# Kernel tuning notes

Measured on AMD Instinct MI355X. Metric: run time of the kernel, lower is better.

The kernel has to match this reference:

```python
import jax, jax.numpy as jnp
import numpy as np


def setup_inputs() -> dict:
    key = jax.random.key(0)
    ks = jax.random.split(key, 16)
    B, S, H = 512, 128, 256
    f32 = jnp.float32
    inputs = jax.random.normal(ks[0], (B, S, 2), f32)
    # xavier-normal-ish init (gain/sqrt(fan_in+fan_out) approximated by small scale)
    def xn(k, shape):
        fan = shape[0] + shape[1]
        return jax.random.normal(k, shape, f32) * np.sqrt(2.0 / fan)
    return {
        "inputs": inputs,
        "W0": xn(ks[1], (H, 2)),   "b0": jnp.zeros((H,), f32),
        "W1": xn(ks[2], (H, H)),   "b1": jnp.zeros((H,), f32),
        "W2": xn(ks[3], (H, H)),   "b2": jnp.zeros((H,), f32),
        "W3": xn(ks[4], (H, H)),   "b3": jnp.zeros((H,), f32),
        "W4": xn(ks[5], (1, H)),   "b4": jnp.zeros((1,), f32),
        "log_growth_rate": jax.random.normal(ks[6], (), f32),
        "log_carrying_capacity": jax.random.normal(ks[7], (), f32),
        "log_initial_loss": jax.random.normal(ks[8], (), f32),
        "in_mean": jnp.array([0.5, 50.0], f32),
        "in_std": jnp.array([0.2, 30.0], f32),
        "tgt_mean": jnp.array([0.8], f32),
        "tgt_std": jnp.array([0.1], f32),
    }


def reference(inputs, W0, b0, W1, b1, W2, b2, W3, b3, W4, b4,
              log_growth_rate, log_carrying_capacity, log_initial_loss,
              in_mean, in_std, tgt_mean, tgt_std):
    B, S = inputs.shape[0], inputs.shape[1]
    # PDE parameters (Verhulst logistic growth)
    r = jnp.exp(-log_growth_rate)
    K = 0.2 + (1.0 - 0.2) * jax.nn.sigmoid(log_carrying_capacity)  # carrying capacity in [0.2, 1]
    C = 0.0 + (0.1 - 0.0) * jax.nn.sigmoid(log_initial_loss)       # initial loss in [0, 0.1]

    # split state feature s and time t, standardize per-column
    s = inputs[..., 0:1].reshape(-1, 1)  # [N,1]
    t = inputs[..., 1:2].reshape(-1, 1)  # [N,1]
    s_norm = (s - in_mean[0:1]) / (in_std[0:1] + 1e-8)
    t_norm = (t - in_mean[1:2]) / (in_std[1:2] + 1e-8)

    Ws = (W0, W1, W2, W3, W4)
    bs = (b0, b1, b2, b3, b4)

    def mlp(x):  # [N,2] -> [N,1], tanh MLP
        h = x
        for W, b in zip(Ws[:-1], bs[:-1]):
            h = jnp.tanh(h @ W.T + b)
        return h @ Ws[-1].T + bs[-1]

    def u_of(tn):  # U(s_norm, tn), inverse-standardized targets
        return mlp(jnp.concatenate([s_norm, tn], axis=-1)) * tgt_std + tgt_mean

    ones = jnp.ones_like(t_norm)

    def uf_of(tn):
        # U and U_t = dU/dt_norm (forward-mode; each point depends on its own scalar t)
        U, U_dot = jax.jvp(u_of, (tn,), (ones,))
        U_t = U_dot.sum(-1, keepdims=True)
        G = r * (U - C) * (1.0 - (U - C) / (K - C))  # Verhulst
        return U, U_t - G  # (U, F)

    # second derivative w.r.t. t_norm: F_t = U_tt - G_t
    (U, F), (_, F_t) = jax.jvp(uf_of, (t_norm,), (ones,))

    shp = (B, S, 1)
    return U.reshape(shp), F.reshape(shp), F_t.reshape(shp)
```

## Files before the change

### kernel.cpp

```cpp
#include <hip/hip_runtime.h>
#include <hip/hip_bf16.h>
#include <math.h>

typedef short s8v __attribute__((ext_vector_type(8)));
typedef float f4v __attribute__((ext_vector_type(4)));

#define HH 256
#define TP 16
#define NTHREADS 256
#define KSTR 520
#define TSTR 4160
#define NTILES 3
#define PLANE (NTILES * TSTR)

__device__ __forceinline__ unsigned short bf_rne(float x){
    union{float f;unsigned u;}v; v.f=x;
    unsigned r = v.u + 0x7FFFu + ((v.u >> 16) & 1u);
    return (unsigned short)(r >> 16);
}
__device__ __forceinline__ unsigned pack_rne2(float a, float b){
    union { __hip_bfloat162 h; unsigned u; } v;
    v.h = __float22bfloat162_rn(float2{a, b});
    return v.u;
}

__global__ __launch_bounds__(256)
void prep_weights(const float* __restrict__ W1, const float* __restrict__ W2,
                  const float* __restrict__ W3, const float* __restrict__ W0,
                  const float* __restrict__ b0, const float* __restrict__ W4,
                  unsigned short* __restrict__ wsB, float* __restrict__ wsF)
{
    int t = blockIdx.x * 256 + threadIdx.x;
    if (t < 24576) {
        int layer = t >> 13;
        int rem = t & 8191;
        int l  = rem & 63;
        int ks = (rem >> 6) & 7;
        int nt = rem >> 9;
        const float* W = (layer == 0) ? W1 : (layer == 1) ? W2 : W3;
        int n_out = nt * 16 + (l & 15);
        int quad  = l >> 4;
        const float* row = W + n_out * HH;
        s8v hi;
        #pragma unroll
        for (int j = 0; j < 8; ++j) {
            int n_in = quad * 64 + (j & 3) * 16 + ((j >> 2) << 3) + ks;
            hi[j] = (short)bf_rne(row[n_in]);
        }
        int dst = ((nt * 8 + ks) * 64 + l) * 8;
        *(s8v*)(wsB + layer * 65536 + dst) = hi;
    } else if (t < 24832) {
        int n = t - 24576;
        int pos = ((n & 7) * 4 + (n >> 6)) * 8 + ((n >> 4) & 3) + 4 * ((n >> 3) & 1);
        wsF[pos]       = W0[2 * n];
        wsF[256 + pos] = W0[2 * n + 1];
        wsF[512 + pos] = b0[n];
        wsF[768 + pos] = W4[n];
    }
}

__global__ __launch_bounds__(NTHREADS, 4)
void capnn_mfma(const float* __restrict__ inp,
                const float* __restrict__ b1, const float* __restrict__ b2,
                const float* __restrict__ b3, const float* __restrict__ b4,
                const float* __restrict__ W4raw,
                const float* __restrict__ lgr, const float* __restrict__ lcc,
                const float* __restrict__ lil,
                const float* __restrict__ imean, const float* __restrict__ istd,
                const float* __restrict__ tmean, const float* __restrict__ tstd,
                const unsigned short* __restrict__ wsW,
                const float* __restrict__ wsF,
                float* __restrict__ out, int N)
{
    __shared__ __align__(16) unsigned short Ahi[PLANE];
    __shared__ float sn_sh[TP], tn_sh[TP];
    __shared__ float head_part[TP * 3 * 4];

    const int tid  = threadIdx.x;
    const int lane = tid & 63;
    const int w    = tid >> 6;
    const int m16  = lane & 15;
    const int q    = lane >> 4;
    const int pbase = blockIdx.x * TP;

    const float* __restrict__ w00p = wsF;
    const float* __restrict__ w01p = wsF + 256;
    const float* __restrict__ b0p  = wsF + 512;

    if (tid < TP) {
        int pg = pbase + tid;
        float s = 0.f, t = 0.f;
        if (pg < N) { s = inp[2 * pg]; t = inp[2 * pg + 1]; }
        sn_sh[tid] = (s - imean[0]) / (istd[0] + 1e-8f);
        tn_sh[tid] = (t - imean[1]) / (istd[1] + 1e-8f);
    }
    __syncthreads();

    {
        const int l  = lane;
        const int p16 = l & 15, quad = l >> 4;
        const float sn = sn_sh[p16], tn = tn_sh[p16];
        #pragma unroll
        for (int g2 = 0; g2 < 2; ++g2) {
            const int ks = w + 4 * g2;
            const int pos = (ks * 4 + quad) * 8;
            float4 wA0 = *(const float4*)(w00p + pos);
            float4 wA1 = *(const float4*)(w00p + pos + 4);
            float4 wB0 = *(const float4*)(w01p + pos);
            float4 wB1 = *(const float4*)(w01p + pos + 4);
            float4 bb0 = *(const float4*)(b0p + pos);
            float4 bb1 = *(const float4*)(b0p + pos + 4);
            float w00v[8] = {wA0.x,wA0.y,wA0.z,wA0.w,wA1.x,wA1.y,wA1.z,wA1.w};
            float w01v[8] = {wB0.x,wB0.y,wB0.z,wB0.w,wB1.x,wB1.y,wB1.z,wB1.w};
            float b0v[8]  = {bb0.x,bb0.y,bb0.z,bb0.w,bb1.x,bb1.y,bb1.z,bb1.w};
            const int base = ks * KSTR + l * 8;
            float av[8], d1v[8], d2v[8];
            #pragma unroll
            for (int j = 0; j < 8; ++j) {
                float z = fmaf(w00v[j], sn, fmaf(w01v[j], tn, b0v[j]));
                float e = __expf(2.f * z);
                float a = 1.f - 2.f * __builtin_amdgcn_rcpf(e + 1.f);
                float g = 1.f - a * a;
                float d1 = g * w01v[j];
                float d2 = -2.f * a * d1 * w01v[j];
                av[j] = a; d1v[j] = d1; d2v[j] = d2;
            }
            #pragma unroll
            for (int s = 0; s < 3; ++s) {
                const float* V = (s == 0) ? av : (s == 1) ? d1v : d2v;
                int4 hi4;
                hi4.x = (int)pack_rne2(V[0], V[1]);
                hi4.y = (int)pack_rne2(V[2], V[3]);
                hi4.z = (int)pack_rne2(V[4], V[5]);
                hi4.w = (int)pack_rne2(V[6], V[7]);
                *(int4*)&Ahi[s * TSTR + base] = hi4;
            }
        }
    }
    __syncthreads();

    for (int L = 0; L < 3; ++L) {
        const unsigned short* __restrict__ Wlh = wsW + L * 65536;
        const float* __restrict__ bL = (L == 0) ? b1 : (L == 1) ? b2 : b3;

        f4v acc[NTILES][4];
        #pragma unroll
        for (int i = 0; i < 4; ++i) {
            float bias = bL[w * 64 + i * 16 + m16];
            acc[0][i] = (f4v){bias, bias, bias, bias};
            acc[1][i] = (f4v){0.f, 0.f, 0.f, 0.f};
            acc[2][i] = (f4v){0.f, 0.f, 0.f, 0.f};
        }

        __builtin_amdgcn_s_setprio(1);
        #pragma unroll
        for (int ks = 0; ks < 8; ++ks) {
            s8v ah[NTILES];
            const int aoff = ks * KSTR + lane * 8;
            #pragma unroll
            for (int t = 0; t < NTILES; ++t)
                ah[t] = *(const s8v*)&Ahi[t * TSTR + aoff];
            #pragma unroll
            for (int i = 0; i < 4; ++i) {
                const int off = (((w * 4 + i) * 8 + ks) * 64 + lane) * 8;
                s8v bh = *(const s8v*)(Wlh + off);
                #pragma unroll
                for (int t = 0; t < NTILES; ++t)
                    acc[t][i] = __builtin_amdgcn_mfma_f32_16x16x32_bf16(ah[t], bh, acc[t][i], 0, 0, 0);
            }
        }
        __builtin_amdgcn_s_setprio(0);

        if (L < 2) {
            __syncthreads();
            const int ksw  = m16 & 7;
            const int hsel = m16 >> 3;
            const int wbase = ksw * KSTR + (16 * w + q * 4) * 8 + 4 * hsel;
            #pragma unroll
            for (int r = 0; r < 4; ++r) {
                float Av[3][4];
                #pragma unroll
                for (int i = 0; i < 4; ++i) {
                    float z  = acc[0][i][r];
                    float z1 = acc[1][i][r];
                    float z2 = acc[2][i][r];
                    float e = __expf(2.f * z);
                    float a = 1.f - 2.f * __builtin_amdgcn_rcpf(e + 1.f);
                    float g = 1.f - a * a;
                    float d1 = g * z1;
                    float d2 = fmaf(g, z2, -2.f * a * d1 * z1);
                    Av[0][i] = a; Av[1][i] = d1; Av[2][i] = d2;
                }
                #pragma unroll
                for (int s = 0; s < 3; ++s) {
                    int2 hi2;
                    hi2.x = (int)pack_rne2(Av[s][0], Av[s][1]);
                    hi2.y = (int)pack_rne2(Av[s][2], Av[s][3]);
                    *(int2*)&Ahi[s * TSTR + wbase + r * 8] = hi2;
                }
            }
            __syncthreads();
        } else {
            float w4v[4];
            #pragma unroll
            for (int i = 0; i < 4; ++i) w4v[i] = W4raw[w * 64 + i * 16 + m16];

            float hp[3][4];
            #pragma unroll
            for (int s = 0; s < 3; ++s)
                #pragma unroll
                for (int r = 0; r < 4; ++r) hp[s][r] = 0.f;
            #pragma unroll
            for (int r = 0; r < 4; ++r) {
                #pragma unroll
                for (int i = 0; i < 4; ++i) {
                    float z  = acc[0][i][r];
                    float z1 = acc[1][i][r];
                    float z2 = acc[2][i][r];
                    float e = __expf(2.f * z);
                    float a = 1.f - 2.f * __builtin_amdgcn_rcpf(e + 1.f);
                    float g = 1.f - a * a;
                    float d1 = g * z1;
                    float d2 = fmaf(g, z2, -2.f * a * d1 * z1);
                    hp[0][r] = fmaf(w4v[i], a,  hp[0][r]);
                    hp[1][r] = fmaf(w4v[i], d1, hp[1][r]);
                    hp[2][r] = fmaf(w4v[i], d2, hp[2][r]);
                }
            }
            #pragma unroll
            for (int m = 1; m < 16; m <<= 1) {
                #pragma unroll
                for (int s = 0; s < 3; ++s)
                    #pragma unroll
                    for (int r = 0; r < 4; ++r)
                        hp[s][r] += __shfl_xor(hp[s][r], m);
            }
            if (m16 == 0) {
                #pragma unroll
                for (int s = 0; s < 3; ++s)
                    #pragma unroll
                    for (int r = 0; r < 4; ++r)
                        head_part[(s * TP + q * 4 + r) * 4 + w] = hp[s][r];
            }
            __syncthreads();
        }
    }

    if (tid < TP) {
        float sv = 0.f, s1v = 0.f, s2v = 0.f;
        #pragma unroll
        for (int ww = 0; ww < 4; ++ww) {
            sv  += head_part[(0 * TP + tid) * 4 + ww];
            s1v += head_part[(1 * TP + tid) * 4 + ww];
            s2v += head_part[(2 * TP + tid) * 4 + ww];
        }
        int pg = pbase + tid;
        if (pg < N) {
            float r_  = expf(-lgr[0]);
            float Kc  = 0.2f + 0.8f / (1.f + expf(-lcc[0]));
            float Cc  = 0.1f / (1.f + expf(-lil[0]));
            float kci = 1.f / (Kc - Cc);
            float ts = tstd[0], tm = tmean[0];
            float U   = (sv + b4[0]) * ts + tm;
            float Ut  = s1v * ts;
            float Utt = s2v * ts;
            float Um  = U - Cc;
            float G   = r_ * Um * (1.f - Um * kci);
            float Gt  = r_ * Ut * (1.f - 2.f * Um * kci);
            out[pg]         = U;
            out[N + pg]     = Ut - G;
            out[2 * N + pg] = Utt - Gt;
        }
    }
}

extern "C" void kernel_launch(void* const* d_in, const int* in_sizes, int n_in,
                              void* d_out, int out_size, void* d_ws, size_t ws_size,
                              hipStream_t stream) {
    const float* inp   = (const float*)d_in[0];
    const float* W0    = (const float*)d_in[1];
    const float* b0    = (const float*)d_in[2];
    const float* W1    = (const float*)d_in[3];
    const float* b1    = (const float*)d_in[4];
    const float* W2    = (const float*)d_in[5];
    const float* b2    = (const float*)d_in[6];
    const float* W3    = (const float*)d_in[7];
    const float* b3    = (const float*)d_in[8];
    const float* W4    = (const float*)d_in[9];
    const float* b4    = (const float*)d_in[10];
    const float* lgr   = (const float*)d_in[11];
    const float* lcc   = (const float*)d_in[12];
    const float* lil   = (const float*)d_in[13];
    const float* imean = (const float*)d_in[14];
    const float* istd  = (const float*)d_in[15];
    const float* tmean = (const float*)d_in[16];
    const float* tstd  = (const float*)d_in[17];

    unsigned short* wsB = (unsigned short*)d_ws;
    float* wsF = (float*)((char*)d_ws + 393216);

    const int N = in_sizes[0] / 2;
    const int gridMain = (N + TP - 1) / TP;

    hipLaunchKernelGGL(prep_weights, dim3(97), dim3(256), 0, stream,
                       W1, W2, W3, W0, b0, W4, wsB, wsF);
    hipLaunchKernelGGL(capnn_mfma, dim3(gridMain), dim3(NTHREADS), 0, stream,
                       inp, b1, b2, b3, b4, W4,
                       lgr, lcc, lil, imean, istd, tmean, tstd,
                       wsB, wsF, (float*)d_out, N);
}
```

Before: 180.4 us.

## Process two point groups per block and interleave MFMA with tanh transforms

Each block now handles 32 points as two 16-point groups with separate LDS planes and accumulators. The layers are software-pipelined so the MFMA work of one group overlaps the tanh/derivative transform of the other. Each layer's weights are also reused across both groups, so B-operand loads per point are halved. In exchange the block uses twice the LDS and more registers, and the occupancy hint drops from 4 to 3 blocks per CU.

```diff
diff --git a/kernel.cpp b/kernel.cpp
--- a/kernel.cpp
+++ b/kernel.cpp
@@ -6,7 +6,7 @@
 typedef float f4v __attribute__((ext_vector_type(4)));
 
 #define HH 256
-#define TP 16
+#define TP 32
 #define NTHREADS 256
 #define KSTR 520
 #define TSTR 4160
@@ -59,7 +59,108 @@
     }
 }
 
-__global__ __launch_bounds__(NTHREADS, 4)
+#define MFMA_LAYER(ACC, PB, WLH, BL) do {                                   \
+    _Pragma("unroll")                                                       \
+    for (int i_ = 0; i_ < 4; ++i_) {                                        \
+        float bias_ = (BL)[w * 64 + i_ * 16 + m16];                         \
+        (ACC)[0][i_] = (f4v){bias_, bias_, bias_, bias_};                   \
+        (ACC)[1][i_] = (f4v){0.f, 0.f, 0.f, 0.f};                           \
+        (ACC)[2][i_] = (f4v){0.f, 0.f, 0.f, 0.f};                           \
+    }                                                                       \
+    __builtin_amdgcn_s_setprio(1);                                          \
+    _Pragma("unroll")                                                       \
+    for (int ks_ = 0; ks_ < 8; ++ks_) {                                     \
+        s8v ah_[NTILES];                                                    \
+        const int aoff_ = (PB) + ks_ * KSTR + lane * 8;                     \
+        _Pragma("unroll")                                                   \
+        for (int t_ = 0; t_ < NTILES; ++t_)                                 \
+            ah_[t_] = *(const s8v*)&Ahi[t_ * TSTR + aoff_];                 \
+        _Pragma("unroll")                                                   \
+        for (int i_ = 0; i_ < 4; ++i_) {                                    \
+            const int off_ = (((w * 4 + i_) * 8 + ks_) * 64 + lane) * 8;    \
+            s8v bh_ = *(const s8v*)((WLH) + off_);                          \
+            _Pragma("unroll")                                               \
+            for (int t_ = 0; t_ < NTILES; ++t_)                             \
+                (ACC)[t_][i_] = __builtin_amdgcn_mfma_f32_16x16x32_bf16(    \
+                    ah_[t_], bh_, (ACC)[t_][i_], 0, 0, 0);                  \
+        }                                                                   \
+    }                                                                       \
+    __builtin_amdgcn_s_setprio(0);                                          \
+} while (0)
+
+#define TRANSFORM(ACC, PB) do {                                             \
+    const int ksw_  = m16 & 7;                                              \
+    const int hsel_ = m16 >> 3;                                             \
+    const int wbase_ = (PB) + ksw_ * KSTR + (16 * w + q * 4) * 8 + 4 * hsel_; \
+    _Pragma("unroll")                                                       \
+    for (int r_ = 0; r_ < 4; ++r_) {                                        \
+        float Av_[3][4];                                                    \
+        _Pragma("unroll")                                                   \
+        for (int i_ = 0; i_ < 4; ++i_) {                                    \
+            float z_  = (ACC)[0][i_][r_];                                   \
+            float z1_ = (ACC)[1][i_][r_];                                   \
+            float z2_ = (ACC)[2][i_][r_];                                   \
+            float e_ = __expf(2.f * z_);                                    \
+            float a_ = 1.f - 2.f * __builtin_amdgcn_rcpf(e_ + 1.f);         \
+            float g_ = 1.f - a_ * a_;                                       \
+            float d1_ = g_ * z1_;                                           \
+            float d2_ = fmaf(g_, z2_, -2.f * a_ * d1_ * z1_);               \
+            Av_[0][i_] = a_; Av_[1][i_] = d1_; Av_[2][i_] = d2_;            \
+        }                                                                   \
+        _Pragma("unroll")                                                   \
+        for (int s_ = 0; s_ < 3; ++s_) {                                    \
+            int2 hi2_;                                                      \
+            hi2_.x = (int)pack_rne2(Av_[s_][0], Av_[s_][1]);                \
+            hi2_.y = (int)pack_rne2(Av_[s_][2], Av_[s_][3]);                \
+            *(int2*)&Ahi[s_ * TSTR + wbase_ + r_ * 8] = hi2_;               \
+        }                                                                   \
+    }                                                                       \
+} while (0)
+
+#define HEAD(ACC, G) do {                                                   \
+    float w4v_[4];                                                          \
+    _Pragma("unroll")                                                       \
+    for (int i_ = 0; i_ < 4; ++i_) w4v_[i_] = W4raw[w * 64 + i_ * 16 + m16];\
+    float hp_[3][4];                                                        \
+    _Pragma("unroll")                                                       \
+    for (int s_ = 0; s_ < 3; ++s_)                                          \
+        _Pragma("unroll")                                                   \
+        for (int r_ = 0; r_ < 4; ++r_) hp_[s_][r_] = 0.f;                   \
+    _Pragma("unroll")                                                       \
+    for (int r_ = 0; r_ < 4; ++r_) {                                        \
+        _Pragma("unroll")                                                   \
+        for (int i_ = 0; i_ < 4; ++i_) {                                    \
+            float z_  = (ACC)[0][i_][r_];                                   \
+            float z1_ = (ACC)[1][i_][r_];                                   \
+            float z2_ = (ACC)[2][i_][r_];                                   \
+            float e_ = __expf(2.f * z_);                                    \
+            float a_ = 1.f - 2.f * __builtin_amdgcn_rcpf(e_ + 1.f);         \
+            float g_ = 1.f - a_ * a_;                                       \
+            float d1_ = g_ * z1_;                                           \
+            float d2_ = fmaf(g_, z2_, -2.f * a_ * d1_ * z1_);               \
+            hp_[0][r_] = fmaf(w4v_[i_], a_,  hp_[0][r_]);                   \
+            hp_[1][r_] = fmaf(w4v_[i_], d1_, hp_[1][r_]);                   \
+            hp_[2][r_] = fmaf(w4v_[i_], d2_, hp_[2][r_]);                   \
+        }                                                                   \
+    }                                                                       \
+    _Pragma("unroll")                                                       \
+    for (int m_ = 1; m_ < 16; m_ <<= 1) {                                   \
+        _Pragma("unroll")                                                   \
+        for (int s_ = 0; s_ < 3; ++s_)                                      \
+            _Pragma("unroll")                                               \
+            for (int r_ = 0; r_ < 4; ++r_)                                  \
+                hp_[s_][r_] += __shfl_xor(hp_[s_][r_], m_);                 \
+    }                                                                       \
+    if (m16 == 0) {                                                         \
+        _Pragma("unroll")                                                   \
+        for (int s_ = 0; s_ < 3; ++s_)                                      \
+            _Pragma("unroll")                                               \
+            for (int r_ = 0; r_ < 4; ++r_)                                  \
+                head_part[G][(s_ * 16 + q * 4 + r_) * 4 + w] = hp_[s_][r_]; \
+    }                                                                       \
+} while (0)
+
+__global__ __launch_bounds__(NTHREADS, 3)
 void capnn_mfma(const float* __restrict__ inp,
                 const float* __restrict__ b1, const float* __restrict__ b2,
                 const float* __restrict__ b3, const float* __restrict__ b4,
@@ -72,9 +173,9 @@
                 const float* __restrict__ wsF,
                 float* __restrict__ out, int N)
 {
-    __shared__ __align__(16) unsigned short Ahi[PLANE];
+    __shared__ __align__(16) unsigned short Ahi[2 * PLANE];
     __shared__ float sn_sh[TP], tn_sh[TP];
-    __shared__ float head_part[TP * 3 * 4];
+    __shared__ float head_part[2][16 * 3 * 4];
 
     const int tid  = threadIdx.x;
     const int lane = tid & 63;
@@ -99,7 +200,6 @@
     {
         const int l  = lane;
         const int p16 = l & 15, quad = l >> 4;
-        const float sn = sn_sh[p16], tn = tn_sh[p16];
         #pragma unroll
         for (int g2 = 0; g2 < 2; ++g2) {
             const int ks = w + 4 * g2;
@@ -114,145 +214,70 @@
             float w01v[8] = {wB0.x,wB0.y,wB0.z,wB0.w,wB1.x,wB1.y,wB1.z,wB1.w};
             float b0v[8]  = {bb0.x,bb0.y,bb0.z,bb0.w,bb1.x,bb1.y,bb1.z,bb1.w};
             const int base = ks * KSTR + l * 8;
-            float av[8], d1v[8], d2v[8];
             #pragma unroll
-            for (int j = 0; j < 8; ++j) {
-                float z = fmaf(w00v[j], sn, fmaf(w01v[j], tn, b0v[j]));
-                float e = __expf(2.f * z);
-                float a = 1.f - 2.f * __builtin_amdgcn_rcpf(e + 1.f);
-                float g = 1.f - a * a;
-                float d1 = g * w01v[j];
-                float d2 = -2.f * a * d1 * w01v[j];
-                av[j] = a; d1v[j] = d1; d2v[j] = d2;
-            }
-            #pragma unroll
-            for (int s = 0; s < 3; ++s) {
-                const float* V = (s == 0) ? av : (s == 1) ? d1v : d2v;
-                int4 hi4;
-                hi4.x = (int)pack_rne2(V[0], V[1]);
-                hi4.y = (int)pack_rne2(V[2], V[3]);
-                hi4.z = (int)pack_rne2(V[4], V[5]);
-                hi4.w = (int)pack_rne2(V[6], V[7]);
-                *(int4*)&Ahi[s * TSTR + base] = hi4;
+            for (int h = 0; h < 2; ++h) {
+                const float sn = sn_sh[h * 16 + p16];
+                const float tn = tn_sh[h * 16 + p16];
+                float av[8], d1v[8], d2v[8];
+                #pragma unroll
+                for (int j = 0; j < 8; ++j) {
+                    float z = fmaf(w00v[j], sn, fmaf(w01v[j], tn, b0v[j]));
+                    float e = __expf(2.f * z);
+                    float a = 1.f - 2.f * __builtin_amdgcn_rcpf(e + 1.f);
+                    float g = 1.f - a * a;
+                    float d1 = g * w01v[j];
+                    float d2 = -2.f * a * d1 * w01v[j];
+                    av[j] = a; d1v[j] = d1; d2v[j] = d2;
+                }
+                #pragma unroll
+                for (int s = 0; s < 3; ++s) {
+                    const float* V = (s == 0) ? av : (s == 1) ? d1v : d2v;
+                    int4 hi4;
+                    hi4.x = (int)pack_rne2(V[0], V[1]);
+                    hi4.y = (int)pack_rne2(V[2], V[3]);
+                    hi4.z = (int)pack_rne2(V[4], V[5]);
+                    hi4.w = (int)pack_rne2(V[6], V[7]);
+                    *(int4*)&Ahi[h * PLANE + s * TSTR + base] = hi4;
+                }
             }
         }
     }
     __syncthreads();
 
-    for (int L = 0; L < 3; ++L) {
-        const unsigned short* __restrict__ Wlh = wsW + L * 65536;
-        const float* __restrict__ bL = (L == 0) ? b1 : (L == 1) ? b2 : b3;
-
-        f4v acc[NTILES][4];
-        #pragma unroll
-        for (int i = 0; i < 4; ++i) {
-            float bias = bL[w * 64 + i * 16 + m16];
-            acc[0][i] = (f4v){bias, bias, bias, bias};
-            acc[1][i] = (f4v){0.f, 0.f, 0.f, 0.f};
-            acc[2][i] = (f4v){0.f, 0.f, 0.f, 0.f};
-        }
-
-        __builtin_amdgcn_s_setprio(1);
-        #pragma unroll
-        for (int ks = 0; ks < 8; ++ks) {
-            s8v ah[NTILES];
-            const int aoff = ks * KSTR + lane * 8;
-            #pragma unroll
-            for (int t = 0; t < NTILES; ++t)
-                ah[t] = *(const s8v*)&Ahi[t * TSTR + aoff];
-            #pragma unroll
-            for (int i = 0; i < 4; ++i) {
-                const int off = (((w * 4 + i) * 8 + ks) * 64 + lane) * 8;
-                s8v bh = *(const s8v*)(Wlh + off);
-                #pragma unroll
-                for (int t = 0; t < NTILES; ++t)
-                    acc[t][i] = __builtin_amdgcn_mfma_f32_16x16x32_bf16(ah[t], bh, acc[t][i], 0, 0, 0);
-            }
-        }
-        __builtin_amdgcn_s_setprio(0);
-
-        if (L < 2) {
-            __syncthreads();
-            const int ksw  = m16 & 7;
-            const int hsel = m16 >> 3;
-            const int wbase = ksw * KSTR + (16 * w + q * 4) * 8 + 4 * hsel;
-            #pragma unroll
-            for (int r = 0; r < 4; ++r) {
-                float Av[3][4];
-                #pragma unroll
-                for (int i = 0; i < 4; ++i) {
-                    float z  = acc[0][i][r];
-                    float z1 = acc[1][i][r];
-                    float z2 = acc[2][i][r];
-                    float e = __expf(2.f * z);
-                    float a = 1.f - 2.f * __builtin_amdgcn_rcpf(e + 1.f);
-                    float g = 1.f - a * a;
-                    float d1 = g * z1;
-                    float d2 = fmaf(g, z2, -2.f * a * d1 * z1);
-                    Av[0][i] = a; Av[1][i] = d1; Av[2][i] = d2;
-                }
-                #pragma unroll
-                for (int s = 0; s < 3; ++s) {
-                    int2 hi2;
-                    hi2.x = (int)pack_rne2(Av[s][0], Av[s][1]);
-                    hi2.y = (int)pack_rne2(Av[s][2], Av[s][3]);
-                    *(int2*)&Ahi[s * TSTR + wbase + r * 8] = hi2;
-                }
-            }
-            __syncthreads();
-        } else {
-            float w4v[4];
-            #pragma unroll
-            for (int i = 0; i < 4; ++i) w4v[i] = W4raw[w * 64 + i * 16 + m16];
-
-            float hp[3][4];
-            #pragma unroll
-            for (int s = 0; s < 3; ++s)
-                #pragma unroll
-                for (int r = 0; r < 4; ++r) hp[s][r] = 0.f;
-            #pragma unroll
-            for (int r = 0; r < 4; ++r) {
-                #pragma unroll
-                for (int i = 0; i < 4; ++i) {
-                    float z  = acc[0][i][r];
-                    float z1 = acc[1][i][r];
-                    float z2 = acc[2][i][r];
-                    float e = __expf(2.f * z);
-                    float a = 1.f - 2.f * __builtin_amdgcn_rcpf(e + 1.f);
-                    float g = 1.f - a * a;
-                    float d1 = g * z1;
-                    float d2 = fmaf(g, z2, -2.f * a * d1 * z1);
-                    hp[0][r] = fmaf(w4v[i], a,  hp[0][r]);
-                    hp[1][r] = fmaf(w4v[i], d1, hp[1][r]);
-                    hp[2][r] = fmaf(w4v[i], d2, hp[2][r]);
-                }
-            }
-            #pragma unroll
-            for (int m = 1; m < 16; m <<= 1) {
-                #pragma unroll
-                for (int s = 0; s < 3; ++s)
-                    #pragma unroll
-                    for (int r = 0; r < 4; ++r)
-                        hp[s][r] += __shfl_xor(hp[s][r], m);
-            }
-            if (m16 == 0) {
-                #pragma unroll
-                for (int s = 0; s < 3; ++s)
-                    #pragma unroll
-                    for (int r = 0; r < 4; ++r)
-                        head_part[(s * TP + q * 4 + r) * 4 + w] = hp[s][r];
-            }
-            __syncthreads();
-        }
-    }
+    f4v accA[NTILES][4], accB[NTILES][4];
+    const unsigned short* __restrict__ W1h = wsW;
+    const unsigned short* __restrict__ W2h = wsW + 65536;
+    const unsigned short* __restrict__ W3h = wsW + 131072;
+
+    MFMA_LAYER(accA, 0, W1h, b1);
+    __syncthreads();
+    MFMA_LAYER(accB, PLANE, W1h, b1);
+    TRANSFORM(accA, 0);
+    __syncthreads();
+    MFMA_LAYER(accA, 0, W2h, b2);
+    TRANSFORM(accB, PLANE);
+    __syncthreads();
+    MFMA_LAYER(accB, PLANE, W2h, b2);
+    TRANSFORM(accA, 0);
+    __syncthreads();
+    MFMA_LAYER(accA, 0, W3h, b3);
+    TRANSFORM(accB, PLANE);
+    __syncthreads();
+    MFMA_LAYER(accB, PLANE, W3h, b3);
+    HEAD(accA, 0);
+    __syncthreads();
+    HEAD(accB, 1);
+    __syncthreads();
 
     if (tid < TP) {
+        const int g = tid >> 4;
+        const int p = tid & 15;
         float sv = 0.f, s1v = 0.f, s2v = 0.f;
         #pragma unroll
         for (int ww = 0; ww < 4; ++ww) {
-            sv  += head_part[(0 * TP + tid) * 4 + ww];
-            s1v += head_part[(1 * TP + tid) * 4 + ww];
-            s2v += head_part[(2 * TP + tid) * 4 + ww];
+            sv  += head_part[g][(0 * 16 + p) * 4 + ww];
+            s1v += head_part[g][(1 * 16 + p) * 4 + ww];
+            s2v += head_part[g][(2 * 16 + p) * 4 + ww];
         }
         int pg = pbase + tid;
         if (pg < N) {
```

New measurement: 195.5 us. +8.4%, slower.

## Double-buffer activation LDS planes and prefetch weight fragments across k-steps

Applied to the files above, without the earlier changes.

Splits the activation tile in shared memory into two ping-pong planes so each layer reads from one plane and writes the next layer's activations to the other. This removes the barrier that used to sit between the MFMA loop and the tanh transform. The MFMA loop now loads the next k-step's weight fragments from global memory before issuing the current step's MFMAs, to hide load latency. Launch bounds drop from 4 to 3 blocks per CU and shared memory per block doubles, which trades occupancy for more registers and fewer syncs.

```diff
diff --git a/kernel.cpp b/kernel.cpp
--- a/kernel.cpp
+++ b/kernel.cpp
@@ -59,7 +59,77 @@
     }
 }
 
-__global__ __launch_bounds__(NTHREADS, 4)
+#define MFMA_LAYER(ACC, RB, WLH, BL) do {                                   \
+    _Pragma("unroll")                                                       \
+    for (int i_ = 0; i_ < 4; ++i_) {                                        \
+        float bias_ = (BL)[w * 64 + i_ * 16 + m16];                         \
+        (ACC)[0][i_] = (f4v){bias_, bias_, bias_, bias_};                   \
+        (ACC)[1][i_] = (f4v){0.f, 0.f, 0.f, 0.f};                          \
+        (ACC)[2][i_] = (f4v){0.f, 0.f, 0.f, 0.f};                          \
+    }                                                                       \
+    s8v bc0_ = *(const s8v*)((WLH) + (((w * 4 + 0) * 8 + 0) * 64 + lane) * 8); \
+    s8v bc1_ = *(const s8v*)((WLH) + (((w * 4 + 1) * 8 + 0) * 64 + lane) * 8); \
+    s8v bc2_ = *(const s8v*)((WLH) + (((w * 4 + 2) * 8 + 0) * 64 + lane) * 8); \
+    s8v bc3_ = *(const s8v*)((WLH) + (((w * 4 + 3) * 8 + 0) * 64 + lane) * 8); \
+    __builtin_amdgcn_s_setprio(1);                                          \
+    _Pragma("unroll")                                                       \
+    for (int ks_ = 0; ks_ < 8; ++ks_) {                                     \
+        const int kn_ = (ks_ < 7) ? ks_ + 1 : ks_;                          \
+        s8v bn0_ = *(const s8v*)((WLH) + (((w * 4 + 0) * 8 + kn_) * 64 + lane) * 8); \
+        s8v bn1_ = *(const s8v*)((WLH) + (((w * 4 + 1) * 8 + kn_) * 64 + lane) * 8); \
+        s8v bn2_ = *(const s8v*)((WLH) + (((w * 4 + 2) * 8 + kn_) * 64 + lane) * 8); \
+        s8v bn3_ = *(const s8v*)((WLH) + (((w * 4 + 3) * 8 + kn_) * 64 + lane) * 8); \
+        const int aoff_ = (RB) + ks_ * KSTR + lane * 8;                     \
+        s8v ah0_ = *(const s8v*)&Ahi[0 * TSTR + aoff_];                     \
+        s8v ah1_ = *(const s8v*)&Ahi[1 * TSTR + aoff_];                     \
+        s8v ah2_ = *(const s8v*)&Ahi[2 * TSTR + aoff_];                     \
+        (ACC)[0][0] = __builtin_amdgcn_mfma_f32_16x16x32_bf16(ah0_, bc0_, (ACC)[0][0], 0, 0, 0); \
+        (ACC)[1][0] = __builtin_amdgcn_mfma_f32_16x16x32_bf16(ah1_, bc0_, (ACC)[1][0], 0, 0, 0); \
+        (ACC)[2][0] = __builtin_amdgcn_mfma_f32_16x16x32_bf16(ah2_, bc0_, (ACC)[2][0], 0, 0, 0); \
+        (ACC)[0][1] = __builtin_amdgcn_mfma_f32_16x16x32_bf16(ah0_, bc1_, (ACC)[0][1], 0, 0, 0); \
+        (ACC)[1][1] = __builtin_amdgcn_mfma_f32_16x16x32_bf16(ah1_, bc1_, (ACC)[1][1], 0, 0, 0); \
+        (ACC)[2][1] = __builtin_amdgcn_mfma_f32_16x16x32_bf16(ah2_, bc1_, (ACC)[2][1], 0, 0, 0); \
+        (ACC)[0][2] = __builtin_amdgcn_mfma_f32_16x16x32_bf16(ah0_, bc2_, (ACC)[0][2], 0, 0, 0); \
+        (ACC)[1][2] = __builtin_amdgcn_mfma_f32_16x16x32_bf16(ah1_, bc2_, (ACC)[1][2], 0, 0, 0); \
+        (ACC)[2][2] = __builtin_amdgcn_mfma_f32_16x16x32_bf16(ah2_, bc2_, (ACC)[2][2], 0, 0, 0); \
+        (ACC)[0][3] = __builtin_amdgcn_mfma_f32_16x16x32_bf16(ah0_, bc3_, (ACC)[0][3], 0, 0, 0); \
+        (ACC)[1][3] = __builtin_amdgcn_mfma_f32_16x16x32_bf16(ah1_, bc3_, (ACC)[1][3], 0, 0, 0); \
+        (ACC)[2][3] = __builtin_amdgcn_mfma_f32_16x16x32_bf16(ah2_, bc3_, (ACC)[2][3], 0, 0, 0); \
+        bc0_ = bn0_; bc1_ = bn1_; bc2_ = bn2_; bc3_ = bn3_;                 \
+    }                                                                       \
+    __builtin_amdgcn_s_setprio(0);                                          \
+} while (0)
+
+#define TRANSFORM(ACC, WB) do {                                             \
+    const int ksw_  = m16 & 7;                                              \
+    const int hsel_ = m16 >> 3;                                             \
+    const int wbase_ = (WB) + ksw_ * KSTR + (16 * w + q * 4) * 8 + 4 * hsel_; \
+    _Pragma("unroll")                                                       \
+    for (int r_ = 0; r_ < 4; ++r_) {                                        \
+        float Av_[3][4];                                                    \
+        _Pragma("unroll")                                                   \
+        for (int i_ = 0; i_ < 4; ++i_) {                                    \
+            float z_  = (ACC)[0][i_][r_];                                   \
+            float z1_ = (ACC)[1][i_][r_];                                   \
+            float z2_ = (ACC)[2][i_][r_];                                   \
+            float e_ = __expf(2.f * z_);                                    \
+            float a_ = 1.f - 2.f * __builtin_amdgcn_rcpf(e_ + 1.f);         \
+            float g_ = 1.f - a_ * a_;                                       \
+            float d1_ = g_ * z1_;                                           \
+            float d2_ = fmaf(g_, z2_, -2.f * a_ * d1_ * z1_);               \
+            Av_[0][i_] = a_; Av_[1][i_] = d1_; Av_[2][i_] = d2_;            \
+        }                                                                   \
+        _Pragma("unroll")                                                   \
+        for (int s_ = 0; s_ < 3; ++s_) {                                    \
+            int2 hi2_;                                                      \
+            hi2_.x = (int)pack_rne2(Av_[s_][0], Av_[s_][1]);                \
+            hi2_.y = (int)pack_rne2(Av_[s_][2], Av_[s_][3]);                \
+            *(int2*)&Ahi[s_ * TSTR + wbase_ + r_ * 8] = hi2_;               \
+        }                                                                   \
+    }                                                                       \
+} while (0)
+
+__global__ __launch_bounds__(NTHREADS, 3)
 void capnn_mfma(const float* __restrict__ inp,
                 const float* __restrict__ b1, const float* __restrict__ b2,
                 const float* __restrict__ b3, const float* __restrict__ b4,
@@ -72,7 +142,7 @@
                 const float* __restrict__ wsF,
                 float* __restrict__ out, int N)
 {
-    __shared__ __align__(16) unsigned short Ahi[PLANE];
+    __shared__ __align__(16) unsigned short Ahi[2 * PLANE];
     __shared__ float sn_sh[TP], tn_sh[TP];
     __shared__ float head_part[TP * 3 * 4];
 
@@ -139,112 +209,64 @@
     }
     __syncthreads();
 
-    for (int L = 0; L < 3; ++L) {
-        const unsigned short* __restrict__ Wlh = wsW + L * 65536;
-        const float* __restrict__ bL = (L == 0) ? b1 : (L == 1) ? b2 : b3;
-
-        f4v acc[NTILES][4];
-        #pragma unroll
-        for (int i = 0; i < 4; ++i) {
-            float bias = bL[w * 64 + i * 16 + m16];
-            acc[0][i] = (f4v){bias, bias, bias, bias};
-            acc[1][i] = (f4v){0.f, 0.f, 0.f, 0.f};
-            acc[2][i] = (f4v){0.f, 0.f, 0.f, 0.f};
-        }
-
-        __builtin_amdgcn_s_setprio(1);
-        #pragma unroll
-        for (int ks = 0; ks < 8; ++ks) {
-            s8v ah[NTILES];
-            const int aoff = ks * KSTR + lane * 8;
-            #pragma unroll
-            for (int t = 0; t < NTILES; ++t)
-                ah[t] = *(const s8v*)&Ahi[t * TSTR + aoff];
+    f4v acc[NTILES][4];
+    const unsigned short* __restrict__ W1h = wsW;
+    const unsigned short* __restrict__ W2h = wsW + 65536;
+    const unsigned short* __restrict__ W3h = wsW + 131072;
+
+    MFMA_LAYER(acc, 0, W1h, b1);
+    TRANSFORM(acc, PLANE);
+    __syncthreads();
+
+    MFMA_LAYER(acc, PLANE, W2h, b2);
+    TRANSFORM(acc, 0);
+    __syncthreads();
+
+    MFMA_LAYER(acc, 0, W3h, b3);
+    {
+        float w4v[4];
+        #pragma unroll
+        for (int i = 0; i < 4; ++i) w4v[i] = W4raw[w * 64 + i * 16 + m16];
+
+        float hp[3][4];
+        #pragma unroll
+        for (int s = 0; s < 3; ++s)
+            #pragma unroll
+            for (int r = 0; r < 4; ++r) hp[s][r] = 0.f;
+        #pragma unroll
+        for (int r = 0; r < 4; ++r) {
             #pragma unroll
             for (int i = 0; i < 4; ++i) {
-                const int off = (((w * 4 + i) * 8 + ks) * 64 + lane) * 8;
-                s8v bh = *(const s8v*)(Wlh + off);
-                #pragma unroll
-                for (int t = 0; t < NTILES; ++t)
-                    acc[t][i] = __builtin_amdgcn_mfma_f32_16x16x32_bf16(ah[t], bh, acc[t][i], 0, 0, 0);
+                float z  = acc[0][i][r];
+                float z1 = acc[1][i][r];
+                float z2 = acc[2][i][r];
+                float e = __expf(2.f * z);
+                float a = 1.f - 2.f * __builtin_amdgcn_rcpf(e + 1.f);
+                float g = 1.f - a * a;
+                float d1 = g * z1;
+                float d2 = fmaf(g, z2, -2.f * a * d1 * z1);
+                hp[0][r] = fmaf(w4v[i], a,  hp[0][r]);
+                hp[1][r] = fmaf(w4v[i], d1, hp[1][r]);
+                hp[2][r] = fmaf(w4v[i], d2, hp[2][r]);
             }
         }
-        __builtin_amdgcn_s_setprio(0);
-
-        if (L < 2) {
-            __syncthreads();
-            const int ksw  = m16 & 7;
-            const int hsel = m16 >> 3;
-            const int wbase = ksw * KSTR + (16 * w + q * 4) * 8 + 4 * hsel;
-            #pragma unroll
-            for (int r = 0; r < 4; ++r) {
-                float Av[3][4];
-                #pragma unroll
-                for (int i = 0; i < 4; ++i) {
-                    float z  = acc[0][i][r];
-                    float z1 = acc[1][i][r];
-                    float z2 = acc[2][i][r];
-                    float e = __expf(2.f * z);
-                    float a = 1.f - 2.f * __builtin_amdgcn_rcpf(e + 1.f);
-                    float g = 1.f - a * a;
-                    float d1 = g * z1;
-                    float d2 = fmaf(g, z2, -2.f * a * d1 * z1);
-                    Av[0][i] = a; Av[1][i] = d1; Av[2][i] = d2;
-                }
-                #pragma unroll
-                for (int s = 0; s < 3; ++s) {
-                    int2 hi2;
-                    hi2.x = (int)pack_rne2(Av[s][0], Av[s][1]);
-                    hi2.y = (int)pack_rne2(Av[s][2], Av[s][3]);
-                    *(int2*)&Ahi[s * TSTR + wbase + r * 8] = hi2;
-                }
-            }
-            __syncthreads();
-        } else {
-            float w4v[4];
-            #pragma unroll
-            for (int i = 0; i < 4; ++i) w4v[i] = W4raw[w * 64 + i * 16 + m16];
-
-            float hp[3][4];
+        #pragma unroll
+        for (int m = 1; m < 16; m <<= 1) {
             #pragma unroll
             for (int s = 0; s < 3; ++s)
                 #pragma unroll
-                for (int r = 0; r < 4; ++r) hp[s][r] = 0.f;
-            #pragma unroll
-            for (int r = 0; r < 4; ++r) {
+                for (int r = 0; r < 4; ++r)
+                    hp[s][r] += __shfl_xor(hp[s][r], m);
+        }
+        if (m16 == 0) {
+            #pragma unroll
+            for (int s = 0; s < 3; ++s)
                 #pragma unroll
-                for (int i = 0; i < 4; ++i) {
-                    float z  = acc[0][i][r];
-                    float z1 = acc[1][i][r];
-                    float z2 = acc[2][i][r];
-                    float e = __expf(2.f * z);
-                    float a = 1.f - 2.f * __builtin_amdgcn_rcpf(e + 1.f);
-                    float g = 1.f - a * a;
-                    float d1 = g * z1;
-                    float d2 = fmaf(g, z2, -2.f * a * d1 * z1);
-                    hp[0][r] = fmaf(w4v[i], a,  hp[0][r]);
-                    hp[1][r] = fmaf(w4v[i], d1, hp[1][r]);
-                    hp[2][r] = fmaf(w4v[i], d2, hp[2][r]);
-                }
-            }
-            #pragma unroll
-            for (int m = 1; m < 16; m <<= 1) {
-                #pragma unroll
-                for (int s = 0; s < 3; ++s)
-                    #pragma unroll
-                    for (int r = 0; r < 4; ++r)
-                        hp[s][r] += __shfl_xor(hp[s][r], m);
-            }
-            if (m16 == 0) {
-                #pragma unroll
-                for (int s = 0; s < 3; ++s)
-                    #pragma unroll
-                    for (int r = 0; r < 4; ++r)
-                        head_part[(s * TP + q * 4 + r) * 4 + w] = hp[s][r];
-            }
-            __syncthreads();
-        }
-    }
+                for (int r = 0; r < 4; ++r)
+                    head_part[(s * TP + q * 4 + r) * 4 + w] = hp[s][r];
+        }
+    }
+    __syncthreads();
 
     if (tid < TP) {
         float sv = 0.f, s1v = 0.f, s2v = 0.f;
```

New measurement: 184.5 us. +2.3%, slower.

## Process two point tiles per block with register-resident weights and staggered transforms

Applied to the files above, without the earlier changes.

Doubles the points per block to 32 and splits them into two halves that share one set of per-layer weight fragments, loaded into registers once. The tanh/derivative transform of one half is interleaved with the MFMA pass of the other half, so ALU work can overlap matrix work and the number of block-wide barriers per half drops. This trades occupancy for more reuse: launch bounds go from 4 to 2 blocks, LDS per block doubles, and the weight fragments hold many registers, which risks spills or less latency hiding.

```diff
diff --git a/kernel.cpp b/kernel.cpp
--- a/kernel.cpp
+++ b/kernel.cpp
@@ -6,11 +6,11 @@
 typedef float f4v __attribute__((ext_vector_type(4)));
 
 #define HH 256
-#define TP 16
+#define TP 32
 #define NTHREADS 256
 #define KSTR 520
 #define TSTR 4160
-#define NTILES 3
+#define NTILES 6
 #define PLANE (NTILES * TSTR)
 
 __device__ __forceinline__ unsigned short bf_rne(float x){
@@ -59,7 +59,113 @@
     }
 }
 
-__global__ __launch_bounds__(NTHREADS, 4)
+template<int H>
+__device__ __forceinline__ void mfma_group(
+    f4v (&acc)[3][4], const s8v (&Bv)[4][8],
+    const unsigned short* Ahi, const float* __restrict__ bL,
+    int lane, int w, int m16)
+{
+    #pragma unroll
+    for (int i = 0; i < 4; ++i) {
+        float bias = bL[w * 64 + i * 16 + m16];
+        acc[0][i] = (f4v){bias, bias, bias, bias};
+        acc[1][i] = (f4v){0.f, 0.f, 0.f, 0.f};
+        acc[2][i] = (f4v){0.f, 0.f, 0.f, 0.f};
+    }
+    __builtin_amdgcn_s_setprio(1);
+    #pragma unroll
+    for (int ks = 0; ks < 8; ++ks) {
+        const int aoff = ks * KSTR + lane * 8;
+        s8v a0 = *(const s8v*)&Ahi[(0 + H) * TSTR + aoff];
+        s8v a1 = *(const s8v*)&Ahi[(2 + H) * TSTR + aoff];
+        s8v a2 = *(const s8v*)&Ahi[(4 + H) * TSTR + aoff];
+        #pragma unroll
+        for (int i = 0; i < 4; ++i) {
+            acc[0][i] = __builtin_amdgcn_mfma_f32_16x16x32_bf16(a0, Bv[i][ks], acc[0][i], 0, 0, 0);
+            acc[1][i] = __builtin_amdgcn_mfma_f32_16x16x32_bf16(a1, Bv[i][ks], acc[1][i], 0, 0, 0);
+            acc[2][i] = __builtin_amdgcn_mfma_f32_16x16x32_bf16(a2, Bv[i][ks], acc[2][i], 0, 0, 0);
+        }
+    }
+    __builtin_amdgcn_s_setprio(0);
+}
+
+template<int H>
+__device__ __forceinline__ void transform_group(
+    f4v (&acc)[3][4], unsigned short* Ahi, int w, int m16, int q)
+{
+    const int ksw  = m16 & 7;
+    const int hsel = m16 >> 3;
+    const int wbase = ksw * KSTR + (16 * w + q * 4) * 8 + 4 * hsel;
+    #pragma unroll
+    for (int r = 0; r < 4; ++r) {
+        float Av[3][4];
+        #pragma unroll
+        for (int i = 0; i < 4; ++i) {
+            float z  = acc[0][i][r];
+            float z1 = acc[1][i][r];
+            float z2 = acc[2][i][r];
+            float e = __expf(2.f * z);
+            float a = 1.f - 2.f * __builtin_amdgcn_rcpf(e + 1.f);
+            float g = 1.f - a * a;
+            float d1 = g * z1;
+            float d2 = fmaf(g, z2, -2.f * a * d1 * z1);
+            Av[0][i] = a; Av[1][i] = d1; Av[2][i] = d2;
+        }
+        #pragma unroll
+        for (int s = 0; s < 3; ++s) {
+            int2 hi2;
+            hi2.x = (int)pack_rne2(Av[s][0], Av[s][1]);
+            hi2.y = (int)pack_rne2(Av[s][2], Av[s][3]);
+            *(int2*)&Ahi[(s * 2 + H) * TSTR + wbase + r * 8] = hi2;
+        }
+    }
+}
+
+template<int H>
+__device__ __forceinline__ void head_group(
+    f4v (&acc)[3][4], const float (&w4v)[4], float* head_part,
+    int w, int m16, int q)
+{
+    float hp[3][4];
+    #pragma unroll
+    for (int s = 0; s < 3; ++s)
+        #pragma unroll
+        for (int r = 0; r < 4; ++r) hp[s][r] = 0.f;
+    #pragma unroll
+    for (int r = 0; r < 4; ++r) {
+        #pragma unroll
+        for (int i = 0; i < 4; ++i) {
+            float z  = acc[0][i][r];
+            float z1 = acc[1][i][r];
+            float z2 = acc[2][i][r];
+            float e = __expf(2.f * z);
+            float a = 1.f - 2.f * __builtin_amdgcn_rcpf(e + 1.f);
+            float g = 1.f - a * a;
+            float d1 = g * z1;
+            float d2 = fmaf(g, z2, -2.f * a * d1 * z1);
+            hp[0][r] = fmaf(w4v[i], a,  hp[0][r]);
+            hp[1][r] = fmaf(w4v[i], d1, hp[1][r]);
+            hp[2][r] = fmaf(w4v[i], d2, hp[2][r]);
+        }
+    }
+    #pragma unroll
+    for (int m = 1; m < 16; m <<= 1) {
+        #pragma unroll
+        for (int s = 0; s < 3; ++s)
+            #pragma unroll
+            for (int r = 0; r < 4; ++r)
+                hp[s][r] += __shfl_xor(hp[s][r], m);
+    }
+    if (m16 == 0) {
+        #pragma unroll
+        for (int s = 0; s < 3; ++s)
+            #pragma unroll
+            for (int r = 0; r < 4; ++r)
+                head_part[(s * TP + H * 16 + q * 4 + r) * 4 + w] = hp[s][r];
+    }
+}
+
+__global__ __launch_bounds__(NTHREADS, 2)
 void capnn_mfma(const float* __restrict__ inp,
                 const float* __restrict__ b1, const float* __restrict__ b2,
                 const float* __restrict__ b3, const float* __restrict__ b4,
@@ -99,7 +205,6 @@
     {
         const int l  = lane;
         const int p16 = l & 15, quad = l >> 4;
-        const float sn = sn_sh[p16], tn = tn_sh[p16];
         #pragma unroll
         for (int g2 = 0; g2 < 2; ++g2) {
             const int ks = w + 4 * g2;
@@ -114,137 +219,77 @@
             float w01v[8] = {wB0.x,wB0.y,wB0.z,wB0.w,wB1.x,wB1.y,wB1.z,wB1.w};
             float b0v[8]  = {bb0.x,bb0.y,bb0.z,bb0.w,bb1.x,bb1.y,bb1.z,bb1.w};
             const int base = ks * KSTR + l * 8;
-            float av[8], d1v[8], d2v[8];
-            #pragma unroll
-            for (int j = 0; j < 8; ++j) {
-                float z = fmaf(w00v[j], sn, fmaf(w01v[j], tn, b0v[j]));
-                float e = __expf(2.f * z);
-                float a = 1.f - 2.f * __builtin_amdgcn_rcpf(e + 1.f);
-                float g = 1.f - a * a;
-                float d1 = g * w01v[j];
-                float d2 = -2.f * a * d1 * w01v[j];
-                av[j] = a; d1v[j] = d1; d2v[j] = d2;
-            }
-            #pragma unroll
-            for (int s = 0; s < 3; ++s) {
-                const float* V = (s == 0) ? av : (s == 1) ? d1v : d2v;
-                int4 hi4;
-                hi4.x = (int)pack_rne2(V[0], V[1]);
-                hi4.y = (int)pack_rne2(V[2], V[3]);
-                hi4.z = (int)pack_rne2(V[4], V[5]);
-                hi4.w = (int)pack_rne2(V[6], V[7]);
-                *(int4*)&Ahi[s * TSTR + base] = hi4;
-            }
-        }
-    }
-    __syncthreads();
-
-    for (int L = 0; L < 3; ++L) {
-        const unsigned short* __restrict__ Wlh = wsW + L * 65536;
-        const float* __restrict__ bL = (L == 0) ? b1 : (L == 1) ? b2 : b3;
-
-        f4v acc[NTILES][4];
-        #pragma unroll
-        for (int i = 0; i < 4; ++i) {
-            float bias = bL[w * 64 + i * 16 + m16];
-            acc[0][i] = (f4v){bias, bias, bias, bias};
-            acc[1][i] = (f4v){0.f, 0.f, 0.f, 0.f};
-            acc[2][i] = (f4v){0.f, 0.f, 0.f, 0.f};
-        }
-
-        __builtin_amdgcn_s_setprio(1);
-        #pragma unroll
-        for (int ks = 0; ks < 8; ++ks) {
-            s8v ah[NTILES];
-            const int aoff = ks * KSTR + lane * 8;
-            #pragma unroll
-            for (int t = 0; t < NTILES; ++t)
-                ah[t] = *(const s8v*)&Ahi[t * TSTR + aoff];
-            #pragma unroll
-            for (int i = 0; i < 4; ++i) {
-                const int off = (((w * 4 + i) * 8 + ks) * 64 + lane) * 8;
-                s8v bh = *(const s8v*)(Wlh + off);
+            #pragma unroll
+            for (int h = 0; h < 2; ++h) {
+                const float sn = sn_sh[h * 16 + p16], tn = tn_sh[h * 16 + p16];
+                float av[8], d1v[8], d2v[8];
                 #pragma unroll
-                for (int t = 0; t < NTILES; ++t)
-                    acc[t][i] = __builtin_amdgcn_mfma_f32_16x16x32_bf16(ah[t], bh, acc[t][i], 0, 0, 0);
-            }
-        }
-        __builtin_amdgcn_s_setprio(0);
-
-        if (L < 2) {
-            __syncthreads();
-            const int ksw  = m16 & 7;
-            const int hsel = m16 >> 3;
-            const int wbase = ksw * KSTR + (16 * w + q * 4) * 8 + 4 * hsel;
-            #pragma unroll
-            for (int r = 0; r < 4; ++r) {
-                float Av[3][4];
-                #pragma unroll
-                for (int i = 0; i < 4; ++i) {
-                    float z  = acc[0][i][r];
-                    float z1 = acc[1][i][r];
-                    float z2 = acc[2][i][r];
+                for (int j = 0; j < 8; ++j) {
+                    float z = fmaf(w00v[j], sn, fmaf(w01v[j], tn, b0v[j]));
                     float e = __expf(2.f * z);
                     float a = 1.f - 2.f * __builtin_amdgcn_rcpf(e + 1.f);
                     float g = 1.f - a * a;
-                    float d1 = g * z1;
-                    float d2 = fmaf(g, z2, -2.f * a * d1 * z1);
-                    Av[0][i] = a; Av[1][i] = d1; Av[2][i] = d2;
+                    float d1 = g * w01v[j];
+                    float d2 = -2.f * a * d1 * w01v[j];
+                    av[j] = a; d1v[j] = d1; d2v[j] = d2;
                 }
                 #pragma unroll
                 for (int s = 0; s < 3; ++s) {
-                    int2 hi2;
-                    hi2.x = (int)pack_rne2(Av[s][0], Av[s][1]);
-                    hi2.y = (int)pack_rne2(Av[s][2], Av[s][3]);
-                    *(int2*)&Ahi[s * TSTR + wbase + r * 8] = hi2;
+                    const float* V = (s == 0) ? av : (s == 1) ? d1v : d2v;
+                    int4 hi4;
+                    hi4.x = (int)pack_rne2(V[0], V[1]);
+                    hi4.y = (int)pack_rne2(V[2], V[3]);
+                    hi4.z = (int)pack_rne2(V[4], V[5]);
+                    hi4.w = (int)pack_rne2(V[6], V[7]);
+                    *(int4*)&Ahi[(s * 2 + h) * TSTR + base] = hi4;
                 }
             }
-            __syncthreads();
-        } else {
-            float w4v[4];
-            #pragma unroll
-            for (int i = 0; i < 4; ++i) w4v[i] = W4raw[w * 64 + i * 16 + m16];
-
-            float hp[3][4];
-            #pragma unroll
-            for (int s = 0; s < 3; ++s)
-                #pragma unroll
-                for (int r = 0; r < 4; ++r) hp[s][r] = 0.f;
-            #pragma unroll
-            for (int r = 0; r < 4; ++r) {
-                #pragma unroll
-                for (int i = 0; i < 4; ++i) {
-                    float z  = acc[0][i][r];
-                    float z1 = acc[1][i][r];
-                    float z2 = acc[2][i][r];
-                    float e = __expf(2.f * z);
-                    float a = 1.f - 2.f * __builtin_amdgcn_rcpf(e + 1.f);
-                    float g = 1.f - a * a;
-                    float d1 = g * z1;
-                    float d2 = fmaf(g, z2, -2.f * a * d1 * z1);
-                    hp[0][r] = fmaf(w4v[i], a,  hp[0][r]);
-                    hp[1][r] = fmaf(w4v[i], d1, hp[1][r]);
-                    hp[2][r] = fmaf(w4v[i], d2, hp[2][r]);
-                }
-            }
-            #pragma unroll
-            for (int m = 1; m < 16; m <<= 1) {
-                #pragma unroll
-                for (int s = 0; s < 3; ++s)
-                    #pragma unroll
-                    for (int r = 0; r < 4; ++r)
-                        hp[s][r] += __shfl_xor(hp[s][r], m);
-            }
-            if (m16 == 0) {
-                #pragma unroll
-                for (int s = 0; s < 3; ++s)
-                    #pragma unroll
-                    for (int r = 0; r < 4; ++r)
-                        head_part[(s * TP + q * 4 + r) * 4 + w] = hp[s][r];
-            }
-            __syncthreads();
-        }
-    }
+        }
+    }
+    __syncthreads();
+
+    f4v acc[3][4];
+
+    #pragma unroll 1
+    for (int L = 0; L < 2; ++L) {
+        const unsigned short* __restrict__ Wlh = wsW + L * 65536;
+        const float* __restrict__ bL = (L == 0) ? b1 : b2;
+
+        s8v Bv[4][8];
+        #pragma unroll
+        for (int i = 0; i < 4; ++i)
+            #pragma unroll
+            for (int ks = 0; ks < 8; ++ks)
+                Bv[i][ks] = *(const s8v*)(Wlh + (((w * 4 + i) * 8 + ks) * 64 + lane) * 8);
+
+        mfma_group<0>(acc, Bv, Ahi, bL, lane, w, m16);
+        __syncthreads();
+        transform_group<0>(acc, Ahi, w, m16, q);
+        mfma_group<1>(acc, Bv, Ahi, bL, lane, w, m16);
+        __syncthreads();
+        transform_group<1>(acc, Ahi, w, m16, q);
+    }
+
+    {
+        const unsigned short* __restrict__ Wlh = wsW + 131072;
+        s8v Bv[4][8];
+        #pragma unroll
+        for (int i = 0; i < 4; ++i)
+            #pragma unroll
+            for (int ks = 0; ks < 8; ++ks)
+                Bv[i][ks] = *(const s8v*)(Wlh + (((w * 4 + i) * 8 + ks) * 64 + lane) * 8);
+
+        float w4v[4];
+        #pragma unroll
+        for (int i = 0; i < 4; ++i) w4v[i] = W4raw[w * 64 + i * 16 + m16];
+
+        mfma_group<0>(acc, Bv, Ahi, b3, lane, w, m16);
+        head_group<0>(acc, w4v, head_part, w, m16, q);
+        __syncthreads();
+        mfma_group<1>(acc, Bv, Ahi, b3, lane, w, m16);
+        head_group<1>(acc, w4v, head_part, w, m16, q);
+    }
+    __syncthreads();
 
     if (tid < TP) {
         float sv = 0.f, s1v = 0.f, s2v = 0.f;
```

New measurement: 173.7 us, median of 2. 1.04x faster.
